# Kernel tuning notes

Measured on AMD Instinct MI355X. Metric: run time of the kernel, lower is better.

Reference implementation:

```python
import jax, jax.numpy as jnp
import numpy as np
import math

D_MODEL = 128      # embedding_dim
D_STATE = 64
D_CONV = 4
NHEADS = 4         # d_inner / headdim (Mamba2 default headdim=64)
HEADDIM = 64
D_INNER = 256      # expand * d_model
CONV_DIM = 384     # d_inner + 2*ngroups*d_state (ngroups=1)
D_IN_PROJ = 644    # 2*d_inner + 2*ngroups*d_state + nheads
NLAYERS = 2
INPUT_DIM = 768
EPS = 1e-5


def setup_inputs() -> dict:
    key = jax.random.key(0)
    ks = jax.random.split(key, 20)
    rn = lambda k, s, sd=0.02: jax.random.normal(k, s, jnp.float32) * sd
    return {
        "x": jax.random.normal(ks[0], (16, 1024, INPUT_DIM), jnp.float32),
        "fc1_W": rn(ks[1], (INPUT_DIM, D_MODEL)),
        "fc1_b": jnp.zeros((D_MODEL,), jnp.float32),
        "ln_w": jnp.ones((NLAYERS, D_MODEL), jnp.float32),
        "ln_b": jnp.zeros((NLAYERS, D_MODEL), jnp.float32),
        "in_W": rn(ks[2], (NLAYERS, D_MODEL, D_IN_PROJ)),
        "conv_w": rn(ks[3], (NLAYERS, D_CONV, CONV_DIM), 0.1),
        "conv_b": jnp.zeros((NLAYERS, CONV_DIM), jnp.float32),
        "dt_bias": rn(ks[4], (NLAYERS, NHEADS), 0.5),
        "A_log": jnp.log(jax.random.uniform(ks[5], (NLAYERS, NHEADS), jnp.float32, 1.0, 16.0)),
        "Dp": jnp.ones((NLAYERS, NHEADS), jnp.float32),
        "rms_w": jnp.ones((NLAYERS, D_INNER), jnp.float32),
        "out_W": rn(ks[6], (NLAYERS, D_INNER, D_MODEL)),
        "fc2_W1": rn(ks[7], (D_MODEL, D_MODEL)),
        "fc2_b1": jnp.zeros((D_MODEL,), jnp.float32),
        "fc2_W2": rn(ks[8], (D_MODEL, 6)),
        "fc2_b2": jnp.zeros((6,), jnp.float32),
    }


def _pos_embedding(L):
    pos = jnp.arange(L, dtype=jnp.float32)[:, None]                       # (L,1)
    div = jnp.exp(jnp.arange(0, D_MODEL, 2, dtype=jnp.float32) * (-math.log(10000.0) / D_MODEL))
    pe = jnp.zeros((L, D_MODEL), jnp.float32)
    pe = pe.at[:, 0::2].set(jnp.sin(pos * div))
    pe = pe.at[:, 1::2].set(jnp.cos(pos * div))
    return pe[None]                                                        # (1,L,D)


def _layernorm(x, w, b):
    mu = jnp.mean(x, -1, keepdims=True)
    var = jnp.mean(jnp.square(x - mu), -1, keepdims=True)
    return (x - mu) * jax.lax.rsqrt(var + EPS) * w + b


def _mamba2(u, in_W, conv_w, conv_b, dt_bias, A_log, Dp, rms_w, out_W):
    b, l, _ = u.shape
    zxbcdt = u @ in_W                                                      # (b,l,644)
    z = zxbcdt[..., :D_INNER]
    xBC = zxbcdt[..., D_INNER:D_INNER + CONV_DIM]
    dt = jax.nn.softplus(zxbcdt[..., D_INNER + CONV_DIM:] + dt_bias)       # (b,l,h)
    # causal depthwise conv1d (width 4) + SiLU
    xp = jnp.pad(xBC, ((0, 0), (D_CONV - 1, 0), (0, 0)))
    xc = conv_b
    for k in range(D_CONV):
        xc = xc + conv_w[k] * xp[:, k:k + l, :]
    xc = jax.nn.silu(xc)                                                   # (b,l,384)
    xh = xc[..., :D_INNER].reshape(b, l, NHEADS, HEADDIM)                  # (b,l,h,p)
    B = xc[..., D_INNER:D_INNER + D_STATE]                                 # (b,l,n)
    C = xc[..., D_INNER + D_STATE:]                                        # (b,l,n)
    A = -jnp.exp(A_log)                                                    # (h,)
    dA = jnp.exp(dt * A)                                                   # (b,l,h)
    dtx = dt[..., None] * xh                                               # (b,l,h,p)

    def step(h, inp):
        dA_t, dtx_t, B_t, C_t = inp                                        # (b,h),(b,h,p),(b,n),(b,n)
        h = dA_t[..., None, None] * h + dtx_t[..., None] * B_t[:, None, None, :]
        y = jnp.einsum('bhpn,bn->bhp', h, C_t)
        return h, y

    h0 = jnp.zeros((b, NHEADS, HEADDIM, D_STATE), u.dtype)
    _, ys = jax.lax.scan(step, h0, (dA.transpose(1, 0, 2), dtx.transpose(1, 0, 2, 3),
                                    B.transpose(1, 0, 2), C.transpose(1, 0, 2)))
    y = ys.transpose(1, 0, 2, 3) + Dp[None, None, :, None] * xh            # (b,l,h,p)
    y = y.reshape(b, l, D_INNER)
    # gated RMSNorm: rmsnorm(y * silu(z)) * weight
    y = y * jax.nn.silu(z)
    y = y * jax.lax.rsqrt(jnp.mean(jnp.square(y), -1, keepdims=True) + EPS) * rms_w
    return y @ out_W


def reference(x, fc1_W, fc1_b, ln_w, ln_b, in_W, conv_w, conv_b, dt_bias,
              A_log, Dp, rms_w, out_W, fc2_W1, fc2_b1, fc2_W2, fc2_b2):
    h = x @ fc1_W + fc1_b                                                  # (b,l,128)
    h = h + _pos_embedding(h.shape[1])
    for i in range(NLAYERS):
        res = h
        hn = _layernorm(h, ln_w[i], ln_b[i])
        h = _mamba2(hn, in_W[i], conv_w[i], conv_b[i], dt_bias[i],
                    A_log[i], Dp[i], rms_w[i], out_W[i]) + res
        # dropout: identity in eval mode
    h = jax.nn.leaky_relu(h @ fc2_W1 + fc2_b1, negative_slope=0.1)
    return h @ fc2_W2 + fc2_b2                                             # (b,l,6)
```

## Files before the change

### kernel.cpp

```cpp
#include <hip/hip_runtime.h>
#include <hip/hip_bf16.h>

#define BATCH 16
#define SEQ 1024
#define NROWS (BATCH*SEQ)
#define IN_DIM 768
#define DM 128
#define DIP 644
#define DI 256
#define CDIM 384
#define DST 64
#define NH 4
#define HD 64
#define CHUNK 64
#define NCHUNK (SEQ/CHUNK)

#define WB_FC1   0
#define WB_IN    98304
#define WB_OUT   263168
#define WB_FC2   328704
#define WB_TOTAL 345088

typedef __attribute__((ext_vector_type(8))) short short8;
typedef __attribute__((ext_vector_type(4))) float float4v;

__device__ __forceinline__ short f2b(float f) {
    unsigned u = __builtin_bit_cast(unsigned, f);
    u += 0x7fffu + ((u >> 16) & 1u);
    return (short)(u >> 16);
}
__device__ __forceinline__ float s2f(short s) {
    unsigned u = ((unsigned)(unsigned short)s) << 16;
    return __builtin_bit_cast(float, u);
}
__device__ __forceinline__ float silu(float a) { return a / (1.f + expf(-a)); }

__global__ void prep_weights(const float* __restrict__ fc1_W, const float* __restrict__ in_W,
                             const float* __restrict__ out_W, const float* __restrict__ fc2_W1,
                             short* __restrict__ wb) {
    int idx = blockIdx.x * 256 + threadIdx.x;
    if (idx < 98304) {
        int n = idx / 768, k = idx % 768;
        wb[WB_FC1 + idx] = f2b(fc1_W[k * 128 + n]);
        return;
    }
    idx -= 98304;
    if (idx < 2 * 82432) {
        int l = idx / 82432, r = idx % 82432;
        int n = r / 128, k = r % 128;
        wb[WB_IN + idx] = f2b(in_W[(size_t)l * 82432 + k * 644 + n]);
        return;
    }
    idx -= 164864;
    if (idx < 2 * 32768) {
        int l = idx / 32768, r = idx % 32768;
        int n = r / 256, k = r % 256;
        wb[WB_OUT + idx] = f2b(out_W[(size_t)l * 32768 + k * 128 + n]);
        return;
    }
    idx -= 65536;
    if (idx < 16384) {
        int n = idx / 128, k = idx % 128;
        wb[WB_FC2 + idx] = f2b(fc2_W1[k * 128 + n]);
    }
}

__global__ __launch_bounds__(512) void fc1_mfma(const float* __restrict__ x,
                                                const short* __restrict__ wt,
                                                const float* __restrict__ bias,
                                                const float* __restrict__ lnw0,
                                                const float* __restrict__ lnb0,
                                                float* __restrict__ h,
                                                short* __restrict__ hnb) {
    __shared__ short As[2][32 * 72];
    __shared__ short Bt[2][128 * 72];
    __shared__ float ps1[32][4], ps2[32][4];
    int tid = threadIdx.x;
    int lane = tid & 63;
    int m = lane & 15;
    int quad = lane >> 4;
    int kq = quad * 8;
    int w = tid >> 6;
    int mrow = (w & 1) * 16;
    int ngrp = w >> 1;
    int ar = tid >> 4;
    int ac = (tid & 15) * 4;
    int row0 = blockIdx.x * 32;
    float4v acc[2];
    acc[0] = (float4v)0.f; acc[1] = (float4v)0.f;

#define FC1_STAGE(BI, KT) { \
        const float* src = x + (size_t)(row0 + ar) * IN_DIM + (KT) * 64 + ac; \
        float4 v = *(const float4*)src; \
        short4 pv; pv.x = f2b(v.x); pv.y = f2b(v.y); pv.z = f2b(v.z); pv.w = f2b(v.w); \
        *reinterpret_cast<short4*>(&As[BI][ar * 72 + ac]) = pv; \
        _Pragma("unroll") \
        for (int i = 0; i < 2; i++) { \
            int idx = tid + i * 512; \
            int n = idx >> 3, kk = (idx & 7) * 8; \
            *reinterpret_cast<short8*>(&Bt[BI][n * 72 + kk]) = \
                *reinterpret_cast<const short8*>(&wt[n * 768 + (KT) * 64 + kk]); \
        } }

    FC1_STAGE(0, 0)
    __syncthreads();
    int buf = 0;
    for (int kt = 0; kt < 12; kt++) {
        int nb = buf ^ 1;
        if (kt < 11) FC1_STAGE(nb, kt + 1)
        short8 a0 = *reinterpret_cast<const short8*>(&As[buf][(mrow + m) * 72 + kq]);
        short8 a1 = *reinterpret_cast<const short8*>(&As[buf][(mrow + m) * 72 + kq + 32]);
        #pragma unroll
        for (int nt = 0; nt < 2; nt++) {
            int bo = (ngrp * 32 + nt * 16 + m) * 72 + kq;
            short8 b0 = *reinterpret_cast<const short8*>(&Bt[buf][bo]);
            short8 b1 = *reinterpret_cast<const short8*>(&Bt[buf][bo + 32]);
            acc[nt] = __builtin_amdgcn_mfma_f32_16x16x32_bf16(a0, b0, acc[nt], 0, 0, 0);
            acc[nt] = __builtin_amdgcn_mfma_f32_16x16x32_bf16(a1, b1, acc[nt], 0, 0, 0);
        }
        __syncthreads();
        buf = nb;
    }
    float val[2][4];
    float s1r[4] = {0.f,0.f,0.f,0.f}, s2r[4] = {0.f,0.f,0.f,0.f};
    #pragma unroll
    for (int nt = 0; nt < 2; nt++) {
        int col = ngrp * 32 + nt * 16 + m;
        float bv = bias[col];
        float div = expf(-(float)(col & ~1) * 0.071955784f);
        #pragma unroll
        for (int r = 0; r < 4; r++) {
            int row = row0 + mrow + quad * 4 + r;
            int t = row & (SEQ - 1);
            float arg = (float)t * div;
            float pe = (col & 1) ? cosf(arg) : sinf(arg);
            float v = acc[nt][r] + bv + pe;
            val[nt][r] = v;
            s1r[r] += v; s2r[r] += v * v;
        }
    }
    #pragma unroll
    for (int o = 1; o < 16; o <<= 1) {
        #pragma unroll
        for (int r = 0; r < 4; r++) {
            s1r[r] += __shfl_xor(s1r[r], o);
            s2r[r] += __shfl_xor(s2r[r], o);
        }
    }
    if (m == 0) {
        #pragma unroll
        for (int r = 0; r < 4; r++) {
            ps1[mrow + quad * 4 + r][ngrp] = s1r[r];
            ps2[mrow + quad * 4 + r][ngrp] = s2r[r];
        }
    }
    __syncthreads();
    #pragma unroll
    for (int r = 0; r < 4; r++) {
        int rl = mrow + quad * 4 + r;
        float s1 = ps1[rl][0] + ps1[rl][1] + ps1[rl][2] + ps1[rl][3];
        float s2 = ps2[rl][0] + ps2[rl][1] + ps2[rl][2] + ps2[rl][3];
        float mu = s1 * (1.f / 128.f);
        float rs = rsqrtf(s2 * (1.f / 128.f) - mu * mu + 1e-5f);
        int row = row0 + rl;
        #pragma unroll
        for (int nt = 0; nt < 2; nt++) {
            int col = ngrp * 32 + nt * 16 + m;
            float v = val[nt][r];
            h[(size_t)row * DM + col] = v;
            hnb[(size_t)row * DM + col] = f2b((v - mu) * rs * lnw0[col] + lnb0[col]);
        }
    }
}

__global__ __launch_bounds__(512) void inproj_mfma(const short* __restrict__ hnb,
                                                   const short* __restrict__ wb,
                                                   short* __restrict__ zb,
                                                   short* __restrict__ xbc,
                                                   int layer) {
    __shared__ short As[64 * 136];
    __shared__ short Bt[128 * 136];
    int tid = threadIdx.x;
    int lane = tid & 63;
    int m = lane & 15;
    int kq = (lane >> 4) * 8;
    int w = tid >> 6;
    int mrow = (w & 3) * 16;
    int ngrp = w >> 2;
    int row0 = blockIdx.x * 64;
    int ncol0 = blockIdx.y * 128;
    const short* wt = wb + WB_IN + (size_t)layer * 82432;
    {
        const short* src = hnb + (size_t)row0 * DM;
        #pragma unroll
        for (int i = 0; i < 2; i++) {
            int u = i * 512 + tid;
            *reinterpret_cast<short8*>(&As[(u >> 4) * 136 + (u & 15) * 8]) =
                *reinterpret_cast<const short8*>(&src[u * 8]);
        }
        #pragma unroll
        for (int i = 0; i < 4; i++) {
            int u = i * 512 + tid;
            int n = u >> 4, c8 = (u & 15) * 8;
            *reinterpret_cast<short8*>(&Bt[n * 136 + c8]) =
                *reinterpret_cast<const short8*>(&wt[(ncol0 + n) * 128 + c8]);
        }
    }
    __syncthreads();
    float4v acc[4];
    acc[0] = (float4v)0.f; acc[1] = (float4v)0.f; acc[2] = (float4v)0.f; acc[3] = (float4v)0.f;
    #pragma unroll
    for (int ks = 0; ks < 4; ks++) {
        short8 a = *reinterpret_cast<const short8*>(&As[(mrow + m) * 136 + ks * 32 + kq]);
        #pragma unroll
        for (int nt = 0; nt < 4; nt++) {
            short8 b = *reinterpret_cast<const short8*>(
                &Bt[(ngrp * 64 + nt * 16 + m) * 136 + ks * 32 + kq]);
            acc[nt] = __builtin_amdgcn_mfma_f32_16x16x32_bf16(a, b, acc[nt], 0, 0, 0);
        }
    }
    int colbase = ncol0 + ngrp * 64;
    if (ncol0 < DI) {
        #pragma unroll
        for (int nt = 0; nt < 4; nt++) {
            int col = colbase + nt * 16 + m;
            #pragma unroll
            for (int r = 0; r < 4; r++) {
                int row = row0 + mrow + (lane >> 4) * 4 + r;
                zb[(size_t)row * DI + col] = f2b(acc[nt][r]);
            }
        }
    } else {
        int xbase = colbase - DI;
        #pragma unroll
        for (int nt = 0; nt < 4; nt++) {
            int col = xbase + nt * 16 + m;
            #pragma unroll
            for (int r = 0; r < 4; r++) {
                int row = row0 + mrow + (lane >> 4) * 4 + r;
                xbc[(size_t)row * CDIM + col] = f2b(acc[nt][r]);
            }
        }
    }
}

__global__ void conv_kernel(const short* __restrict__ xbc,
                            const float* __restrict__ convw, const float* __restrict__ convb,
                            short* __restrict__ xcb,
                            const short* __restrict__ hnb, const short* __restrict__ wb,
                            const float* __restrict__ dt_bias, float* __restrict__ dtb,
                            int layer) {
    int c = threadIdx.x;
    int row0 = blockIdx.x * 4;
    int l0 = row0 & (SEQ - 1);
    const float* cw = convw + (size_t)layer * 4 * CDIM;
    float w0 = cw[c], w1 = cw[CDIM + c], w2 = cw[2 * CDIM + c], w3 = cw[3 * CDIM + c];
    float bb = convb[layer * CDIM + c];
    float v[7];
    #pragma unroll
    for (int i = 0; i < 7; i++) {
        int rr = row0 + i - 3;
        v[i] = (l0 + i - 3 >= 0) ? s2f(xbc[(size_t)rr * CDIM + c]) : 0.f;
    }
    #pragma unroll
    for (int j = 0; j < 4; j++) {
        float acc = bb + w0 * v[j] + w1 * v[j + 1] + w2 * v[j + 2] + w3 * v[j + 3];
        xcb[(size_t)(row0 + j) * CDIM + c] = f2b(silu(acc));
    }
    if (c < 128) {
        int r = c >> 5;
        int rem = c & 31;
        int hh = rem >> 3;
        int part = rem & 7;
        const short* hrow = hnb + (size_t)(row0 + r) * DM + part * 16;
        const short* wrow = wb + WB_IN + (size_t)layer * 82432 + (640 + hh) * 128 + part * 16;
        short8 hv0 = *reinterpret_cast<const short8*>(hrow);
        short8 hv1 = *reinterpret_cast<const short8*>(hrow + 8);
        short8 wv0 = *reinterpret_cast<const short8*>(wrow);
        short8 wv1 = *reinterpret_cast<const short8*>(wrow + 8);
        float s = 0.f;
        #pragma unroll
        for (int q = 0; q < 8; q++)
            s += s2f(hv0[q]) * s2f(wv0[q]) + s2f(hv1[q]) * s2f(wv1[q]);
        s += __shfl_xor(s, 1);
        s += __shfl_xor(s, 2);
        s += __shfl_xor(s, 4);
        if (part == 0) {
            float raw = s + dt_bias[layer * NH + hh];
            float dt = (raw > 20.f) ? raw : log1pf(expf(raw));
            dtb[(size_t)(row0 + r) * NH + hh] = dt;
        }
    }
}

__global__ __launch_bounds__(256) void chunk_state_mfma(const short* __restrict__ xcb,
                                                        const float* __restrict__ dtb,
                                                        const float* __restrict__ A_log,
                                                        short* __restrict__ Slocb,
                                                        float* __restrict__ decay, int layer) {
    __shared__ short XTw[64 * 72];
    __shared__ short BT[64 * 72];
    __shared__ float wst[64];
    int bid = blockIdx.x;
    int c  = bid & (NCHUNK - 1);
    int hh = (bid >> 4) & (NH - 1);
    int b  = bid >> 6;
    int tid = threadIdx.x;
    int row0 = b * SEQ + c * CHUNK;
    float A = -expf(A_log[layer * NH + hh]);

    if (tid < CHUNK) {
        float dtv = dtb[(size_t)(row0 + tid) * NH + hh];
        float l = dtv * A;
        #pragma unroll
        for (int o = 1; o < 64; o <<= 1) { float v = __shfl_up(l, o); if (tid >= o) l += v; }
        float Ltot = __shfl(l, 63);
        wst[tid] = expf(Ltot - l) * dtv;
        if (tid == 63) decay[bid] = expf(Ltot);
    }
    __syncthreads();
    {
        int p = tid & 63;
        int tb0 = tid >> 6;
        #pragma unroll
        for (int i = 0; i < 2; i++) {
            int t0 = (tb0 + i * 4) * 8;
            short8 xv, bv;
            #pragma unroll
            for (int j = 0; j < 8; j++) {
                int t = t0 + j;
                const short* xr = xcb + (size_t)(row0 + t) * CDIM;
                xv[j] = f2b(s2f(xr[hh * HD + p]) * wst[t]);
                bv[j] = xr[DI + p];
            }
            *reinterpret_cast<short8*>(&XTw[p * 72 + t0]) = xv;
            *reinterpret_cast<short8*>(&BT[p * 72 + t0]) = bv;
        }
    }
    __syncthreads();

    int lane = tid & 63;
    int m = lane & 15;
    int kq = (lane >> 4) * 8;
    int w = tid >> 6;
    int a_off = (w * 16 + m) * 72 + kq;
    float4v acc[4];
    acc[0] = (float4v)0.f; acc[1] = (float4v)0.f; acc[2] = (float4v)0.f; acc[3] = (float4v)0.f;
    short8 a0 = *reinterpret_cast<const short8*>(&XTw[a_off]);
    short8 a1 = *reinterpret_cast<const short8*>(&XTw[a_off + 32]);
    #pragma unroll
    for (int nt = 0; nt < 4; nt++) {
        int bo = (nt * 16 + m) * 72 + kq;
        short8 b0 = *reinterpret_cast<const short8*>(&BT[bo]);
        short8 b1 = *reinterpret_cast<const short8*>(&BT[bo + 32]);
        acc[nt] = __builtin_amdgcn_mfma_f32_16x16x32_bf16(a0, b0, acc[nt], 0, 0, 0);
        acc[nt] = __builtin_amdgcn_mfma_f32_16x16x32_bf16(a1, b1, acc[nt], 0, 0, 0);
    }
    short* Sp = Slocb + (size_t)bid * (HD * DST);
    int tq = (lane >> 4) * 4;
    #pragma unroll
    for (int nt = 0; nt < 4; nt++) {
        #pragma unroll
        for (int r = 0; r < 4; r++) {
            int p = w * 16 + tq + r;
            int n = nt * 16 + m;
            Sp[p * DST + n] = f2b(acc[nt][r]);
        }
    }
}

__global__ __launch_bounds__(256) void chunk_out_mfma(const short* __restrict__ xcb,
                                                      const float* __restrict__ dtb,
                                                      const float* __restrict__ A_log,
                                                      const float* __restrict__ Dpw,
                                                      const short* __restrict__ Slocb,
                                                      const float* __restrict__ decay,
                                                      short* __restrict__ ybb, int layer) {
    __shared__ short Cb[64 * 72];
    __shared__ short Bb[64 * 72];
    __shared__ short XT[64 * 72];
    __shared__ short HT[64 * 72];
    __shared__ float Ls[64], dts[64];
    int bid = blockIdx.x;
    int c  = bid & (NCHUNK - 1);
    int hh = (bid >> 4) & (NH - 1);
    int b  = bid >> 6;
    int tid = threadIdx.x;
    int row0 = b * SEQ + c * CHUNK;
    int bh0 = bid & ~(NCHUNK - 1);
    float A = -expf(A_log[layer * NH + hh]);
    float Dph = Dpw[layer * NH + hh];

    if (tid < CHUNK) {
        float dtv = dtb[(size_t)(row0 + tid) * NH + hh];
        float l = dtv * A;
        #pragma unroll
        for (int o = 1; o < 64; o <<= 1) { float v = __shfl_up(l, o); if (tid >= o) l += v; }
        Ls[tid] = l;
        dts[tid] = dtv;
    }
    {
        float hreg[16];
        #pragma unroll
        for (int k = 0; k < 16; k++) hreg[k] = 0.f;
        for (int j = 0; j < c; j++) {
            float d = decay[bh0 + j];
            const short* Sp = Slocb + (size_t)(bh0 + j) * (HD * DST) + tid * 16;
            short8 s0 = *reinterpret_cast<const short8*>(Sp);
            short8 s1 = *reinterpret_cast<const short8*>(Sp + 8);
            #pragma unroll
            for (int k = 0; k < 8; k++) {
                hreg[k]     = d * hreg[k]     + s2f(s0[k]);
                hreg[8 + k] = d * hreg[8 + k] + s2f(s1[k]);
            }
        }
        int p = tid >> 2;
        int n0 = (tid & 3) * 16;
        short8 h0, h1;
        #pragma unroll
        for (int k = 0; k < 8; k++) { h0[k] = f2b(hreg[k]); h1[k] = f2b(hreg[8 + k]); }
        *reinterpret_cast<short8*>(&HT[p * 72 + n0]) = h0;
        *reinterpret_cast<short8*>(&HT[p * 72 + n0 + 8]) = h1;
    }
    {
        int p = tid & 63;
        int tb0 = tid >> 6;
        #pragma unroll
        for (int i = 0; i < 2; i++) {
            int t0 = (tb0 + i * 4) * 8;
            short8 xv;
            #pragma unroll
            for (int j = 0; j < 8; j++)
                xv[j] = xcb[(size_t)(row0 + t0 + j) * CDIM + hh * HD + p];
            *reinterpret_cast<short8*>(&XT[p * 72 + t0]) = xv;
        }
    }
    #pragma unroll
    for (int i = 0; i < 2; i++) {
        int idx = tid + i * 256;
        int t = idx >> 3, cb = (idx & 7) * 8;
        const short* xr = xcb + (size_t)(row0 + t) * CDIM;
        *reinterpret_cast<short8*>(&Bb[t * 72 + cb]) =
            *reinterpret_cast<const short8*>(&xr[DI + cb]);
        *reinterpret_cast<short8*>(&Cb[t * 72 + cb]) =
            *reinterpret_cast<const short8*>(&xr[DI + DST + cb]);
    }
    __syncthreads();

    int lane = tid & 63;
    int m = lane & 15;
    int kq = (lane >> 4) * 8;
    int w = tid >> 6;
    int tq = (lane >> 4) * 4;
    int a_off = (w * 16 + m) * 72 + kq;

    short8 ca0 = *reinterpret_cast<const short8*>(&Cb[a_off]);
    short8 ca1 = *reinterpret_cast<const short8*>(&Cb[a_off + 32]);

    float4v g[4], ir[4];
    #pragma unroll
    for (int i = 0; i < 4; i++) { g[i] = (float4v)0.f; ir[i] = (float4v)0.f; }
    #pragma unroll
    for (int st = 0; st < 4; st++) {
        int bo = (st * 16 + m) * 72 + kq;
        short8 b0 = *reinterpret_cast<const short8*>(&Bb[bo]);
        short8 b1 = *reinterpret_cast<const short8*>(&Bb[bo + 32]);
        g[st] = __builtin_amdgcn_mfma_f32_16x16x32_bf16(ca0, b0, g[st], 0, 0, 0);
        g[st] = __builtin_amdgcn_mfma_f32_16x16x32_bf16(ca1, b1, g[st], 0, 0, 0);
        short8 h0 = *reinterpret_cast<const short8*>(&HT[bo]);
        short8 h1 = *reinterpret_cast<const short8*>(&HT[bo + 32]);
        ir[st] = __builtin_amdgcn_mfma_f32_16x16x32_bf16(ca0, h0, ir[st], 0, 0, 0);
        ir[st] = __builtin_amdgcn_mfma_f32_16x16x32_bf16(ca1, h1, ir[st], 0, 0, 0);
    }
    __syncthreads();
    #pragma unroll
    for (int st = 0; st < 4; st++) {
        #pragma unroll
        for (int r = 0; r < 4; r++) {
            int t = w * 16 + tq + r;
            int s = st * 16 + m;
            float mv = 0.f;
            if (s <= t) mv = g[st][r] * expf(Ls[t] - Ls[s]) * dts[s];
            Bb[t * 72 + s] = f2b(mv);
        }
    }
    __syncthreads();
    float4v yi[4];
    #pragma unroll
    for (int i = 0; i < 4; i++) yi[i] = (float4v)0.f;
    short8 ma0 = *reinterpret_cast<const short8*>(&Bb[a_off]);
    short8 ma1 = *reinterpret_cast<const short8*>(&Bb[a_off + 32]);
    #pragma unroll
    for (int pt = 0; pt < 4; pt++) {
        int bo = (pt * 16 + m) * 72 + kq;
        short8 x0 = *reinterpret_cast<const short8*>(&XT[bo]);
        short8 x1 = *reinterpret_cast<const short8*>(&XT[bo + 32]);
        yi[pt] = __builtin_amdgcn_mfma_f32_16x16x32_bf16(ma0, x0, yi[pt], 0, 0, 0);
        yi[pt] = __builtin_amdgcn_mfma_f32_16x16x32_bf16(ma1, x1, yi[pt], 0, 0, 0);
    }
    #pragma unroll
    for (int r = 0; r < 4; r++) {
        int t = w * 16 + tq + r;
        float et = expf(Ls[t]);
        short* yr = ybb + (size_t)(row0 + t) * DI + hh * HD;
        #pragma unroll
        for (int pt = 0; pt < 4; pt++) {
            int p = pt * 16 + m;
            float xv = s2f(XT[p * 72 + t]);
            yr[p] = f2b(yi[pt][r] + et * ir[pt][r] + Dph * xv);
        }
    }
}

__global__ __launch_bounds__(512) void outproj_gate_mfma(const short* __restrict__ ybb,
                                                         const short* __restrict__ zb,
                                                         const float* __restrict__ rmsw,
                                                         const short* __restrict__ wb,
                                                         const float* __restrict__ lnw2,
                                                         const float* __restrict__ lnb2,
                                                         float* __restrict__ h,
                                                         short* __restrict__ hnb,
                                                         const float* __restrict__ fc2_b1,
                                                         const float* __restrict__ fc2_W2,
                                                         const float* __restrict__ fc2_b2,
                                                         float* __restrict__ outp,
                                                         int layer, int do_fc2) {
    __shared__ __align__(16) short As[32 * 264];
    __shared__ __align__(16) short Bt[2][128 * 72];
    __shared__ float w2s[768];
    int tid = threadIdx.x;
    int lane = tid & 63;
    int m = lane & 15;
    int quad = lane >> 4;
    int kq = quad * 8;
    int w = tid >> 6;
    int mrow = (w & 1) * 16;
    int ngrp = w >> 1;
    int row0 = blockIdx.x * 32;
    const short* wt = wb + WB_OUT + (size_t)layer * 32768;
    if (do_fc2)
        for (int i = tid; i < 768; i += 512) w2s[i] = fc2_W2[i];
    {
        int r = tid >> 4, j = tid & 15;
        const short* yr = ybb + (size_t)(row0 + r) * DI + j * 16;
        const short* zr = zb + (size_t)(row0 + r) * DI + j * 16;
        short8 y0 = *reinterpret_cast<const short8*>(yr);
        short8 y1 = *reinterpret_cast<const short8*>(yr + 8);
        short8 z0 = *reinterpret_cast<const short8*>(zr);
        short8 z1 = *reinterpret_cast<const short8*>(zr + 8);
        float v[16]; float s2 = 0.f;
        #pragma unroll
        for (int q = 0; q < 8; q++) {
            v[q]     = s2f(y0[q]) * silu(s2f(z0[q]));
            v[8 + q] = s2f(y1[q]) * silu(s2f(z1[q]));
        }
        #pragma unroll
        for (int q = 0; q < 16; q++) s2 += v[q] * v[q];
        #pragma unroll
        for (int o = 1; o < 16; o <<= 1) s2 += __shfl_xor(s2, o);
        float rs = rsqrtf(s2 * (1.f / 256.f) + 1e-5f);
        const float* rw = rmsw + layer * DI + j * 16;
        short8 a0, a1;
        #pragma unroll
        for (int q = 0; q < 8; q++) {
            a0[q] = f2b(v[q] * rs * rw[q]);
            a1[q] = f2b(v[8 + q] * rs * rw[8 + q]);
        }
        *reinterpret_cast<short8*>(&As[r * 264 + j * 16]) = a0;
        *reinterpret_cast<short8*>(&As[r * 264 + j * 16 + 8]) = a1;
    }
    {
        int n = tid >> 2, kk = (tid & 3) * 16;
        *reinterpret_cast<short8*>(&Bt[0][n * 72 + kk]) =
            *reinterpret_cast<const short8*>(&wt[n * 256 + kk]);
        *reinterpret_cast<short8*>(&Bt[0][n * 72 + kk + 8]) =
            *reinterpret_cast<const short8*>(&wt[n * 256 + kk + 8]);
    }
    __syncthreads();
    float4v acc[2];
    acc[0] = (float4v)0.f; acc[1] = (float4v)0.f;
    int buf = 0;
    for (int kt = 0; kt < 4; kt++) {
        if (kt < 3) {
            int n = tid >> 2, kk = (tid & 3) * 16;
            *reinterpret_cast<short8*>(&Bt[buf ^ 1][n * 72 + kk]) =
                *reinterpret_cast<const short8*>(&wt[n * 256 + (kt + 1) * 64 + kk]);
            *reinterpret_cast<short8*>(&Bt[buf ^ 1][n * 72 + kk + 8]) =
                *reinterpret_cast<const short8*>(&wt[n * 256 + (kt + 1) * 64 + kk + 8]);
        }
        short8 a0 = *reinterpret_cast<const short8*>(&As[(mrow + m) * 264 + kt * 64 + kq]);
        short8 a1 = *reinterpret_cast<const short8*>(&As[(mrow + m) * 264 + kt * 64 + kq + 32]);
        #pragma unroll
        for (int nt = 0; nt < 2; nt++) {
            int bo = (ngrp * 32 + nt * 16 + m) * 72 + kq;
            short8 b0 = *reinterpret_cast<const short8*>(&Bt[buf][bo]);
            short8 b1 = *reinterpret_cast<const short8*>(&Bt[buf][bo + 32]);
            acc[nt] = __builtin_amdgcn_mfma_f32_16x16x32_bf16(a0, b0, acc[nt], 0, 0, 0);
            acc[nt] = __builtin_amdgcn_mfma_f32_16x16x32_bf16(a1, b1, acc[nt], 0, 0, 0);
        }
        __syncthreads();
        buf ^= 1;
    }
    float* hs = (float*)As;
    #pragma unroll
    for (int nt = 0; nt < 2; nt++) {
        int col = ngrp * 32 + nt * 16 + m;
        #pragma unroll
        for (int r = 0; r < 4; r++)
            hs[(mrow + quad * 4 + r) * 132 + col] = acc[nt][r];
    }
    __syncthreads();
    int er = tid >> 4, ej = tid & 15;
    int erow = row0 + er;
    float vals[8];
    float s1 = 0.f, s2v = 0.f;
    {
        const float* hsrc = h + (size_t)erow * DM + ej * 8;
        float4 h0 = *(const float4*)hsrc;
        float4 h1 = *(const float4*)(hsrc + 4);
        const float* hrow = &hs[er * 132 + ej * 8];
        float4 q0 = *(const float4*)hrow;
        float4 q1 = *(const float4*)(hrow + 4);
        vals[0] = h0.x + q0.x; vals[1] = h0.y + q0.y; vals[2] = h0.z + q0.z; vals[3] = h0.w + q0.w;
        vals[4] = h1.x + q1.x; vals[5] = h1.y + q1.y; vals[6] = h1.z + q1.z; vals[7] = h1.w + q1.w;
        #pragma unroll
        for (int i = 0; i < 8; i++) { s1 += vals[i]; s2v += vals[i] * vals[i]; }
    }
    if (!do_fc2) {
        #pragma unroll
        for (int o = 1; o < 16; o <<= 1) { s1 += __shfl_xor(s1, o); s2v += __shfl_xor(s2v, o); }
        float* hdst = h + (size_t)erow * DM + ej * 8;
        *(float4*)hdst = make_float4(vals[0], vals[1], vals[2], vals[3]);
        *(float4*)(hdst + 4) = make_float4(vals[4], vals[5], vals[6], vals[7]);
        float mu = s1 * (1.f / 128.f);
        float rs2 = rsqrtf(s2v * (1.f / 128.f) - mu * mu + 1e-5f);
        const float* lw = lnw2 + ej * 8;
        const float* lb = lnb2 + ej * 8;
        short8 a0;
        #pragma unroll
        for (int i = 0; i < 8; i++) a0[i] = f2b((vals[i] - mu) * rs2 * lw[i] + lb[i]);
        *reinterpret_cast<short8*>(hnb + (size_t)erow * DM + ej * 8) = a0;
        return;
    }
    __syncthreads();
    short* As2 = (short*)As;
    {
        short8 ap;
        #pragma unroll
        for (int i = 0; i < 8; i++) ap[i] = f2b(vals[i]);
        *reinterpret_cast<short8*>(&As2[er * 136 + ej * 8]) = ap;
    }
    const short* wtf = wb + WB_FC2;
    short* Bt2 = (short*)Bt;
    {
        int n = tid >> 2, kk = (tid & 3) * 32;
        #pragma unroll
        for (int i = 0; i < 4; i++)
            *reinterpret_cast<short8*>(&Bt2[n * 136 + kk + i * 8]) =
                *reinterpret_cast<const short8*>(&wtf[n * 128 + kk + i * 8]);
    }
    __syncthreads();
    float4v acc2[2];
    acc2[0] = (float4v)0.f; acc2[1] = (float4v)0.f;
    #pragma unroll
    for (int kt = 0; kt < 2; kt++) {
        int k0 = kt * 64;
        short8 a0 = *reinterpret_cast<const short8*>(&As2[(mrow + m) * 136 + k0 + kq]);
        short8 a1 = *reinterpret_cast<const short8*>(&As2[(mrow + m) * 136 + k0 + kq + 32]);
        #pragma unroll
        for (int nt = 0; nt < 2; nt++) {
            int bo = (ngrp * 32 + nt * 16 + m) * 136 + k0 + kq;
            short8 b0 = *reinterpret_cast<const short8*>(&Bt2[bo]);
            short8 b1 = *reinterpret_cast<const short8*>(&Bt2[bo + 32]);
            acc2[nt] = __builtin_amdgcn_mfma_f32_16x16x32_bf16(a0, b0, acc2[nt], 0, 0, 0);
            acc2[nt] = __builtin_amdgcn_mfma_f32_16x16x32_bf16(a1, b1, acc2[nt], 0, 0, 0);
        }
    }
    __syncthreads();
    float* h2s = (float*)As;
    #pragma unroll
    for (int nt = 0; nt < 2; nt++) {
        int col = ngrp * 32 + nt * 16 + m;
        float bv = fc2_b1[col];
        #pragma unroll
        for (int r = 0; r < 4; r++) {
            float o = acc2[nt][r] + bv;
            h2s[(mrow + quad * 4 + r) * 132 + col] = (o > 0.f) ? o : 0.1f * o;
        }
    }
    __syncthreads();
    if (tid < 384) {
        int r = tid / 12, q = tid % 12, cc = q >> 1, part = q & 1;
        float a2 = 0.f;
        #pragma unroll 8
        for (int k = 0; k < 64; k++)
            a2 += h2s[r * 132 + part * 64 + k] * w2s[(part * 64 + k) * 6 + cc];
        a2 += __shfl_xor(a2, 1);
        if (!part) outp[(size_t)(row0 + r) * 6 + cc] = fc2_b2[cc] + a2;
    }
}

extern "C" void kernel_launch(void* const* d_in, const int* in_sizes, int n_in,
                              void* d_out, int out_size, void* d_ws, size_t ws_size,
                              hipStream_t stream) {
    const float* x       = (const float*)d_in[0];
    const float* fc1_W   = (const float*)d_in[1];
    const float* fc1_b   = (const float*)d_in[2];
    const float* ln_w    = (const float*)d_in[3];
    const float* ln_b    = (const float*)d_in[4];
    const float* in_W    = (const float*)d_in[5];
    const float* conv_w  = (const float*)d_in[6];
    const float* conv_b  = (const float*)d_in[7];
    const float* dt_bias = (const float*)d_in[8];
    const float* A_log   = (const float*)d_in[9];
    const float* Dp      = (const float*)d_in[10];
    const float* rms_w   = (const float*)d_in[11];
    const float* out_W   = (const float*)d_in[12];
    const float* fc2_W1  = (const float*)d_in[13];
    const float* fc2_b1  = (const float*)d_in[14];
    const float* fc2_W2  = (const float*)d_in[15];
    const float* fc2_b2  = (const float*)d_in[16];
    float* out = (float*)d_out;

    float* ws = (float*)d_ws;
    float* h     = ws;
    float* dtb   = h     + (size_t)NROWS * DM;
    float* decay = dtb   + (size_t)NROWS * NH;
    short* sbase = (short*)(decay + 1024);
    short* hnb   = sbase;
    short* zb    = hnb   + (size_t)NROWS * DM;
    short* xbc   = zb    + (size_t)NROWS * DI;
    short* xcb   = xbc   + (size_t)NROWS * CDIM;
    short* ybb   = xcb   + (size_t)NROWS * CDIM;
    short* Slocb = ybb   + (size_t)NROWS * DI;
    short* wb    = Slocb + (size_t)BATCH*NH*NCHUNK*HD*DST;

    prep_weights<<<1348, 256, 0, stream>>>(fc1_W, in_W, out_W, fc2_W1, wb);
    fc1_mfma<<<NROWS / 32, 512, 0, stream>>>(x, wb + WB_FC1, fc1_b, ln_w, ln_b, h, hnb);

    for (int layer = 0; layer < 2; layer++) {
        inproj_mfma<<<dim3(NROWS / 64, 5), 512, 0, stream>>>(hnb, wb, zb, xbc, layer);
        conv_kernel<<<NROWS / 4, CDIM, 0, stream>>>(xbc, conv_w, conv_b, xcb,
                                                    hnb, wb, dt_bias, dtb, layer);
        chunk_state_mfma<<<BATCH*NH*NCHUNK, 256, 0, stream>>>(xcb, dtb, A_log, Slocb, decay, layer);
        chunk_out_mfma<<<BATCH*NH*NCHUNK, 256, 0, stream>>>(xcb, dtb, A_log, Dp, Slocb, decay,
                                                            ybb, layer);
        outproj_gate_mfma<<<NROWS / 32, 512, 0, stream>>>(ybb, zb, rms_w, wb,
                                                          ln_w + DM, ln_b + DM, h, hnb,
                                                          fc2_b1, fc2_W2, fc2_b2, out,
                                                          layer, layer == 1 ? 1 : 0);
    }
}
```

Baseline: 245.0 us.

## Precompute inter-chunk states with a separate sequential scan kernel

Previously each chunk_out block recomputed the carried state by looping over all earlier chunks, which is quadratic in chunk count and means reading up to 15 chunk states per block. A new state_scan kernel (one block per batch-head) runs the recurrence once and writes the prefix state for every chunk, and chunk_out then just loads its state. This adds a kernel launch plus a small 64-block serial scan that underuses the GPU, and extra workspace for Hpre.

```diff
diff --git a/kernel.cpp b/kernel.cpp
--- a/kernel.cpp
+++ b/kernel.cpp
@@ -369,12 +369,44 @@
     }
 }
 
+__global__ __launch_bounds__(256) void state_scan(const short* __restrict__ Slocb,
+                                                  const float* __restrict__ decay,
+                                                  short* __restrict__ Hpre) {
+    int sid = blockIdx.x;
+    int tid = threadIdx.x;
+    size_t base = (size_t)sid * NCHUNK * (HD * DST);
+    float hreg[16];
+    #pragma unroll
+    for (int k = 0; k < 16; k++) hreg[k] = 0.f;
+    {
+        short8 z = (short8)0;
+        *reinterpret_cast<short8*>(Hpre + base + tid * 16) = z;
+        *reinterpret_cast<short8*>(Hpre + base + tid * 16 + 8) = z;
+    }
+    for (int c = 1; c < NCHUNK; c++) {
+        float d = decay[sid * NCHUNK + c - 1];
+        const short* Sp = Slocb + base + (size_t)(c - 1) * (HD * DST) + tid * 16;
+        short8 s0 = *reinterpret_cast<const short8*>(Sp);
+        short8 s1 = *reinterpret_cast<const short8*>(Sp + 8);
+        short8 h0, h1;
+        #pragma unroll
+        for (int k = 0; k < 8; k++) {
+            hreg[k]     = d * hreg[k]     + s2f(s0[k]);
+            hreg[8 + k] = d * hreg[8 + k] + s2f(s1[k]);
+            h0[k] = f2b(hreg[k]);
+            h1[k] = f2b(hreg[8 + k]);
+        }
+        short* Hp = Hpre + base + (size_t)c * (HD * DST) + tid * 16;
+        *reinterpret_cast<short8*>(Hp) = h0;
+        *reinterpret_cast<short8*>(Hp + 8) = h1;
+    }
+}
+
 __global__ __launch_bounds__(256) void chunk_out_mfma(const short* __restrict__ xcb,
                                                       const float* __restrict__ dtb,
                                                       const float* __restrict__ A_log,
                                                       const float* __restrict__ Dpw,
-                                                      const short* __restrict__ Slocb,
-                                                      const float* __restrict__ decay,
+                                                      const short* __restrict__ Hpre,
                                                       short* __restrict__ ybb, int layer) {
     __shared__ short Cb[64 * 72];
     __shared__ short Bb[64 * 72];
@@ -387,9 +419,9 @@
     int b  = bid >> 6;
     int tid = threadIdx.x;
     int row0 = b * SEQ + c * CHUNK;
-    int bh0 = bid & ~(NCHUNK - 1);
     float A = -expf(A_log[layer * NH + hh]);
     float Dph = Dpw[layer * NH + hh];
+    (void)c;
 
     if (tid < CHUNK) {
         float dtv = dtb[(size_t)(row0 + tid) * NH + hh];
@@ -400,25 +432,11 @@
         dts[tid] = dtv;
     }
     {
-        float hreg[16];
-        #pragma unroll
-        for (int k = 0; k < 16; k++) hreg[k] = 0.f;
-        for (int j = 0; j < c; j++) {
-            float d = decay[bh0 + j];
-            const short* Sp = Slocb + (size_t)(bh0 + j) * (HD * DST) + tid * 16;
-            short8 s0 = *reinterpret_cast<const short8*>(Sp);
-            short8 s1 = *reinterpret_cast<const short8*>(Sp + 8);
-            #pragma unroll
-            for (int k = 0; k < 8; k++) {
-                hreg[k]     = d * hreg[k]     + s2f(s0[k]);
-                hreg[8 + k] = d * hreg[8 + k] + s2f(s1[k]);
-            }
-        }
+        const short* Hp = Hpre + (size_t)bid * (HD * DST) + tid * 16;
+        short8 h0 = *reinterpret_cast<const short8*>(Hp);
+        short8 h1 = *reinterpret_cast<const short8*>(Hp + 8);
         int p = tid >> 2;
         int n0 = (tid & 3) * 16;
-        short8 h0, h1;
-        #pragma unroll
-        for (int k = 0; k < 8; k++) { h0[k] = f2b(hreg[k]); h1[k] = f2b(hreg[8 + k]); }
         *reinterpret_cast<short8*>(&HT[p * 72 + n0]) = h0;
         *reinterpret_cast<short8*>(&HT[p * 72 + n0 + 8]) = h1;
     }
@@ -733,7 +751,8 @@
     short* xcb   = xbc   + (size_t)NROWS * CDIM;
     short* ybb   = xcb   + (size_t)NROWS * CDIM;
     short* Slocb = ybb   + (size_t)NROWS * DI;
-    short* wb    = Slocb + (size_t)BATCH*NH*NCHUNK*HD*DST;
+    short* Hpre  = Slocb + (size_t)BATCH*NH*NCHUNK*HD*DST;
+    short* wb    = Hpre  + (size_t)BATCH*NH*NCHUNK*HD*DST;
 
     prep_weights<<<1348, 256, 0, stream>>>(fc1_W, in_W, out_W, fc2_W1, wb);
     fc1_mfma<<<NROWS / 32, 512, 0, stream>>>(x, wb + WB_FC1, fc1_b, ln_w, ln_b, h, hnb);
@@ -743,7 +762,8 @@
         conv_kernel<<<NROWS / 4, CDIM, 0, stream>>>(xbc, conv_w, conv_b, xcb,
                                                     hnb, wb, dt_bias, dtb, layer);
         chunk_state_mfma<<<BATCH*NH*NCHUNK, 256, 0, stream>>>(xcb, dtb, A_log, Slocb, decay, layer);
-        chunk_out_mfma<<<BATCH*NH*NCHUNK, 256, 0, stream>>>(xcb, dtb, A_log, Dp, Slocb, decay,
+        state_scan<<<BATCH*NH, 256, 0, stream>>>(Slocb, decay, Hpre);
+        chunk_out_mfma<<<BATCH*NH*NCHUNK, 256, 0, stream>>>(xcb, dtb, A_log, Dp, Hpre,
                                                             ybb, layer);
         outproj_gate_mfma<<<NROWS / 32, 512, 0, stream>>>(ybb, zb, rms_w, wb,
                                                           ln_w + DM, ln_b + DM, h, hnb,
```

Result: no change. 248.1 us (+1.3%).
